# Kernel tuning notes

Hardware: AMD Instinct MI355X
Metric: run time of the kernel (lower is better)

The kernel has to match this reference:

```python
import jax, jax.numpy as jnp
import numpy as np

B = 262144      # batch
DIN = 100       # input covariate dim (cfg_density[0][0])
H = 64          # hidden dim
G = 10          # num_grid -> density output dim G+1
NH = 5          # number of dosage-bucket heads in Multi_head


def setup_inputs() -> dict:
    key = jax.random.key(0)
    ks = jax.random.split(key, 16)
    s = 0.05
    return {
        "dosage": jax.random.uniform(ks[0], (B,), dtype=jnp.float32),
        "x": jax.random.normal(ks[1], (B, DIN), dtype=jnp.float32),
        # density feature MLP (two Linear+ReLU layers)
        "dW0": jax.random.normal(ks[2], (DIN, H), dtype=jnp.float32) * s,
        "db0": jax.random.normal(ks[3], (H,), dtype=jnp.float32) * s,
        "dW1": jax.random.normal(ks[4], (H, H), dtype=jnp.float32) * s,
        "db1": jax.random.normal(ks[5], (H,), dtype=jnp.float32) * s,
        # Density_Block: Linear(H -> G+1) then softmax + grid interpolation
        "dbW": jax.random.normal(ks[6], (H, G + 1), dtype=jnp.float32) * s,
        "dbB": jax.random.normal(ks[7], (G + 1,), dtype=jnp.float32) * s,
        # Multi_head: 5 structurally identical heads, params stacked on axis 0
        # layer0: Treat_Linear(64 -> 64, relu, istreat=1)
        "W0": jax.random.normal(ks[8], (NH, H, H), dtype=jnp.float32) * s,
        "tw0": jax.random.normal(ks[9], (NH, H), dtype=jnp.float32) * s,
        "b0": jax.random.normal(ks[10], (NH, H), dtype=jnp.float32) * s,
        # layer1 (last): Treat_Linear(64 -> 1, no act, istreat=1)
        "W1": jax.random.normal(ks[11], (NH, H, 1), dtype=jnp.float32) * s,
        "tw1": jax.random.normal(ks[12], (NH, 1), dtype=jnp.float32) * s,
        "b1": jax.random.normal(ks[13], (NH, 1), dtype=jnp.float32) * s,
    }


def reference(dosage, x, dW0, db0, dW1, db1, dbW, dbB, W0, tw0, b0, W1, tw1, b1):
    # hidden feature MLP
    hidden = jax.nn.relu(x @ dW0 + db0)
    hidden = jax.nn.relu(hidden @ dW1 + db1)            # [B, H]

    # ---- Density_Block: softmax over grid, dual gather + linear interpolation
    p = jax.nn.softmax(hidden @ dbW + dbB, axis=1)      # [B, G+1]
    tB = dosage * G
    U = jnp.ceil(tB)
    inter = 1.0 - (U - tB)                              # fractional position in cell
    Ui = U.astype(jnp.int32)
    Li = Ui - 1
    Li = Li + (Li < 0).astype(jnp.int32)                # clamp L=-1 -> 0
    pL = jnp.take_along_axis(p, Li[:, None], axis=1)[:, 0]
    pU = jnp.take_along_axis(p, Ui[:, None], axis=1)[:, 0]
    g = pL + (pU - pL) * inter                          # [B]

    # ---- Multi_head: 5 heads on dosage buckets [0,.2),[.2,.4),...,[.8,1.)
    t = dosage
    # layer0: out = feat @ W + t * tw + b, relu; compute all heads, select later
    h0 = jax.nn.relu(
        jnp.einsum('bi,hio->bho', hidden, W0)
        + t[:, None, None] * tw0[None]
        + b0[None]
    )                                                   # [B, NH, H]
    # last layer: no activation
    out1 = (jnp.einsum('bho,hoj->bhj', h0, W1)
            + t[:, None, None] * tw1[None]
            + b1[None])                                 # [B, NH, 1]
    bucket = jnp.clip(jnp.floor(t * NH).astype(jnp.int32), 0, NH - 1)
    Q = jnp.take_along_axis(out1, bucket[:, None, None], axis=1)[:, 0, :]  # [B, 1]
    return g, Q
```

## Files before the change

kernel.cpp:

```cpp
#include <hip/hip_runtime.h>

typedef __attribute__((ext_vector_type(8))) short  short8;
typedef __attribute__((ext_vector_type(4))) float  floatx4;
typedef __attribute__((ext_vector_type(4))) int    intx4;

constexpr int DIN = 100;
constexpr int H   = 64;
constexpr int G   = 10;
constexpr int NH  = 5;
constexpr int MWG = 128;
constexpr int HP  = 72;

constexpr int NF_DW0 = 16, NF_DW1 = 8, NF_DBW = 2;
constexpr int NF_LIN = NF_DW0 + NF_DW1 + NF_DBW;
constexpr int NF_TOT = NF_LIN + 40;

__device__ __forceinline__ unsigned short f2bf_rne(float f) {
    union { float f; unsigned u; } v{f};
    unsigned r = v.u + 0x7FFF + ((v.u >> 16) & 1);
    return (unsigned short)(r >> 16);
}

__device__ __forceinline__ short8 pack8(const float* f) {
    intx4 p;
    #pragma unroll
    for (int j = 0; j < 4; ++j) {
        unsigned a = __float_as_uint(f[2 * j])     + 0x8000u;
        unsigned b = __float_as_uint(f[2 * j + 1]) + 0x8000u;
        p[j] = (int)((b & 0xFFFF0000u) | (a >> 16));
    }
    union { intx4 i; short8 s; } u; u.i = p;
    return u.s;
}

__device__ __forceinline__ unsigned short f2bf_hu(float f) {
    return (unsigned short)((__float_as_uint(f) + 0x8000u) >> 16);
}

__device__ __forceinline__ short8 ldfrag(const unsigned short* __restrict__ ws,
                                         int f, int lane) {
    return *(const short8*)(ws + (size_t)(f * 64 + lane) * 8);
}

__global__ __launch_bounds__(64) void pack_kernel(
    const float* __restrict__ dW0, const float* __restrict__ dW1,
    const float* __restrict__ dbW, const float* __restrict__ W0,
    unsigned short* __restrict__ ws)
{
    const int f = blockIdx.x;
    const int lane = threadIdx.x;
    const int q = lane >> 4, cl = lane & 15;
    float v[8];
    if (f < NF_DW0) {
        int c = f >> 2, g = f & 3;
        #pragma unroll
        for (int j = 0; j < 8; ++j) {
            int k = c * 32 + q * 8 + j, n = g * 16 + cl;
            v[j] = (k < DIN) ? dW0[k * H + n] : 0.0f;
        }
    } else if (f < NF_DW0 + NF_DW1) {
        int r = f - NF_DW0; int c = r >> 2, g = r & 3;
        #pragma unroll
        for (int j = 0; j < 8; ++j) {
            int k = c * 32 + q * 8 + j, n = g * 16 + cl;
            v[j] = dW1[k * H + n];
        }
    } else if (f < NF_LIN) {
        int c = f - (NF_DW0 + NF_DW1);
        #pragma unroll
        for (int j = 0; j < 8; ++j) {
            int k = c * 32 + q * 8 + j, n = cl;
            v[j] = (n <= G) ? dbW[k * (G + 1) + n] : 0.0f;
        }
    } else {
        int r = f - NF_LIN; int h = r >> 3; r &= 7; int c = r >> 2, g = r & 3;
        #pragma unroll
        for (int j = 0; j < 8; ++j) {
            int k = c * 32 + q * 8 + j, n = g * 16 + cl;
            v[j] = W0[(h * H + k) * H + n];
        }
    }
    short8 s;
    #pragma unroll
    for (int j = 0; j < 8; ++j) s[j] = (short)f2bf_rne(v[j]);
    *(short8*)(ws + (size_t)(f * 64 + lane) * 8) = s;
}

__global__ __launch_bounds__(256, 4) void drnet_mfma(
    const float* __restrict__ dosage, const float* __restrict__ x,
    const float* __restrict__ db0, const float* __restrict__ db1,
    const float* __restrict__ dbB,
    const float* __restrict__ tw0, const float* __restrict__ b0,
    const float* __restrict__ W1, const float* __restrict__ tw1,
    const float* __restrict__ b1,
    const unsigned short* __restrict__ wsfrag,
    float* __restrict__ outg, float* __restrict__ outq)
{
    __shared__ unsigned short hbuf[MWG * HP];
    const int tid  = threadIdx.x;
    const int wave = tid >> 6, lane = tid & 63;
    const int q = lane >> 4, cl = lane & 15;
    const int rowbase = blockIdx.x * MWG + wave * 32;
    unsigned short* hb = hbuf + wave * 32 * HP;

    float t8[2][4];
    int   bk8[2][4];
    #pragma unroll
    for (int mt = 0; mt < 2; ++mt) {
        floatx4 tv = *(const floatx4*)(dosage + rowbase + mt * 16 + 4 * q);
        #pragma unroll
        for (int r = 0; r < 4; ++r) {
            float t = tv[r];
            t8[mt][r] = t;
            int bk = (int)floorf(t * (float)NH);
            bk8[mt][r] = min(max(bk, 0), NH - 1);
        }
    }

    #pragma unroll 1
    for (int mt = 0; mt < 2; ++mt) {
        short8 a1[4];
        const float* xr = x + (size_t)(rowbase + mt * 16 + cl) * DIN;
        #pragma unroll
        for (int cch = 0; cch < 4; ++cch) {
            float f[8];
            if (cch < 3) {
                floatx4 u0 = *(const floatx4*)(xr + cch * 32 + q * 8);
                floatx4 u1 = *(const floatx4*)(xr + cch * 32 + q * 8 + 4);
                f[0]=u0.x; f[1]=u0.y; f[2]=u0.z; f[3]=u0.w;
                f[4]=u1.x; f[5]=u1.y; f[6]=u1.z; f[7]=u1.w;
            } else {
                if (q == 0) {
                    floatx4 u0 = *(const floatx4*)(xr + 96);
                    f[0]=u0.x; f[1]=u0.y; f[2]=u0.z; f[3]=u0.w;
                    f[4]=f[5]=f[6]=f[7]=0.0f;
                } else {
                    #pragma unroll
                    for (int j = 0; j < 8; ++j) f[j] = 0.0f;
                }
            }
            a1[cch] = pack8(f);
        }
        floatx4 acc[4];
        #pragma unroll
        for (int g = 0; g < 4; ++g) acc[g] = (floatx4)0.0f;
        #pragma unroll
        for (int cch = 0; cch < 4; ++cch)
            #pragma unroll
            for (int g = 0; g < 4; ++g) {
                short8 bf = ldfrag(wsfrag, cch * 4 + g, lane);
                acc[g] = __builtin_amdgcn_mfma_f32_16x16x32_bf16(a1[cch], bf, acc[g], 0, 0, 0);
            }
        #pragma unroll
        for (int g = 0; g < 4; ++g) {
            float bias = db0[g * 16 + cl];
            #pragma unroll
            for (int r = 0; r < 4; ++r)
                hb[(mt * 16 + 4 * q + r) * HP + g * 16 + cl] =
                    f2bf_hu(fmaxf(acc[g][r] + bias, 0.0f));
        }
    }

    #pragma unroll 1
    for (int mt = 0; mt < 2; ++mt) {
        short8 a2[2];
        #pragma unroll
        for (int cch = 0; cch < 2; ++cch)
            a2[cch] = *(const short8*)(hb + (mt * 16 + cl) * HP + cch * 32 + q * 8);
        floatx4 acc[4];
        #pragma unroll
        for (int g = 0; g < 4; ++g) acc[g] = (floatx4)0.0f;
        #pragma unroll
        for (int cch = 0; cch < 2; ++cch)
            #pragma unroll
            for (int g = 0; g < 4; ++g) {
                short8 bf = ldfrag(wsfrag, NF_DW0 + cch * 4 + g, lane);
                acc[g] = __builtin_amdgcn_mfma_f32_16x16x32_bf16(a2[cch], bf, acc[g], 0, 0, 0);
            }
        #pragma unroll
        for (int g = 0; g < 4; ++g) {
            float bias = db1[g * 16 + cl];
            #pragma unroll
            for (int r = 0; r < 4; ++r)
                hb[(mt * 16 + 4 * q + r) * HP + g * 16 + cl] =
                    f2bf_hu(fmaxf(acc[g][r] + bias, 0.0f));
        }
    }

    short8 af[2][2];
    #pragma unroll
    for (int mt = 0; mt < 2; ++mt)
        #pragma unroll
        for (int cch = 0; cch < 2; ++cch)
            af[mt][cch] = *(const short8*)(hb + (mt * 16 + cl) * HP + cch * 32 + q * 8);

    {
        floatx4 accd[2];
        accd[0] = (floatx4)0.0f; accd[1] = (floatx4)0.0f;
        #pragma unroll
        for (int cch = 0; cch < 2; ++cch) {
            short8 bf = ldfrag(wsfrag, NF_DW0 + NF_DW1 + cch, lane);
            #pragma unroll
            for (int mt = 0; mt < 2; ++mt)
                accd[mt] = __builtin_amdgcn_mfma_f32_16x16x32_bf16(af[mt][cch], bf, accd[mt], 0, 0, 0);
        }
        const float dbBv = (cl <= G) ? dbB[cl] : 0.0f;
        #pragma unroll
        for (int mt = 0; mt < 2; ++mt) {
            float gout[4];
            #pragma unroll
            for (int r = 0; r < 4; ++r) {
                float e = (cl <= G) ? __expf(accd[mt][r] + dbBv) : 0.0f;
                float s = e;
                s += __shfl_xor(s, 1); s += __shfl_xor(s, 2);
                s += __shfl_xor(s, 4); s += __shfl_xor(s, 8);
                const float t  = t8[mt][r];
                const float tB = t * (float)G;
                const float U  = ceilf(tB);
                const float inter = 1.0f - (U - tB);
                int Ui = (int)U; int Li = Ui - 1; if (Li < 0) Li = 0;
                float pL = __shfl(e, q * 16 + Li);
                float pU = __shfl(e, q * 16 + Ui);
                gout[r] = (pL + (pU - pL) * inter) / s;
            }
            if (cl == 0) {
                floatx4 gv = { gout[0], gout[1], gout[2], gout[3] };
                *(floatx4*)(outg + rowbase + mt * 16 + 4 * q) = gv;
            }
        }
    }

    float qp[2][4] = {{0,0,0,0},{0,0,0,0}};
    #pragma unroll 1
    for (int h = 0; h < NH; ++h) {
        #pragma unroll
        for (int gh = 0; gh < 2; ++gh) {
            floatx4 acch[2][2];
            #pragma unroll
            for (int mt = 0; mt < 2; ++mt)
                #pragma unroll
                for (int g = 0; g < 2; ++g) acch[mt][g] = (floatx4)0.0f;
            #pragma unroll
            for (int cch = 0; cch < 2; ++cch)
                #pragma unroll
                for (int g = 0; g < 2; ++g) {
                    short8 bf = ldfrag(wsfrag, NF_LIN + h * 8 + cch * 4 + gh * 2 + g, lane);
                    #pragma unroll
                    for (int mt = 0; mt < 2; ++mt)
                        acch[mt][g] = __builtin_amdgcn_mfma_f32_16x16x32_bf16(af[mt][cch], bf, acch[mt][g], 0, 0, 0);
                }
            #pragma unroll
            for (int g = 0; g < 2; ++g) {
                const int off = h * H + (gh * 2 + g) * 16 + cl;
                const float tw0v = tw0[off], b0v = b0[off], w1v = W1[off];
                #pragma unroll
                for (int mt = 0; mt < 2; ++mt)
                    #pragma unroll
                    for (int r = 0; r < 4; ++r) {
                        float h0 = acch[mt][g][r] + t8[mt][r] * tw0v + b0v;
                        float c  = fmaxf(h0, 0.0f) * w1v;
                        qp[mt][r] += (bk8[mt][r] == h) ? c : 0.0f;
                    }
            }
        }
    }
    #pragma unroll
    for (int mt = 0; mt < 2; ++mt) {
        #pragma unroll
        for (int r = 0; r < 4; ++r) {
            float s = qp[mt][r];
            s += __shfl_xor(s, 1); s += __shfl_xor(s, 2);
            s += __shfl_xor(s, 4); s += __shfl_xor(s, 8);
            const int h = bk8[mt][r];
            qp[mt][r] = s + t8[mt][r] * tw1[h] + b1[h];
        }
        if (cl == 0) {
            floatx4 Qv = { qp[mt][0], qp[mt][1], qp[mt][2], qp[mt][3] };
            *(floatx4*)(outq + rowbase + mt * 16 + 4 * q) = Qv;
        }
    }
}

extern "C" void kernel_launch(void* const* d_in, const int* in_sizes, int n_in,
                              void* d_out, int out_size, void* d_ws, size_t ws_size,
                              hipStream_t stream) {
    const float* dosage = (const float*)d_in[0];
    const float* x      = (const float*)d_in[1];
    const float* dW0    = (const float*)d_in[2];
    const float* db0    = (const float*)d_in[3];
    const float* dW1    = (const float*)d_in[4];
    const float* db1    = (const float*)d_in[5];
    const float* dbW    = (const float*)d_in[6];
    const float* dbB    = (const float*)d_in[7];
    const float* W0     = (const float*)d_in[8];
    const float* tw0    = (const float*)d_in[9];
    const float* b0     = (const float*)d_in[10];
    const float* W1     = (const float*)d_in[11];
    const float* tw1    = (const float*)d_in[12];
    const float* b1     = (const float*)d_in[13];

    const int Btot = in_sizes[0];
    float* outg = (float*)d_out;
    float* outq = outg + Btot;
    unsigned short* ws = (unsigned short*)d_ws;

    pack_kernel<<<NF_TOT, 64, 0, stream>>>(dW0, dW1, dbW, W0, ws);
    drnet_mfma<<<Btot / MWG, 256, 0, stream>>>(dosage, x, db0, db1, dbB,
                                               tw0, b0, W1, tw1, b1,
                                               ws, outg, outq);
}
```

Before: 201.5 us.

## Bucket rows by dosage head so each row evaluates only its own head

Adds a scatter kernel that sorts row indices into per-head lists using shared-memory and global atomics. A new bucketed kernel then processes each head's rows, gathering x rows by index and running only that head's layer-0 MFMAs instead of all five. This removes the redundant head computation, which was the bulk of the MFMA work. In exchange it adds a memset, a scatter pass, non-contiguous gathers and scattered output writes, and it launches many blocks that exit immediately. It falls back to the old kernel when the workspace is too small.

```diff
diff --git a/kernel.cpp b/kernel.cpp
--- a/kernel.cpp
+++ b/kernel.cpp
@@ -84,6 +84,219 @@
     #pragma unroll
     for (int j = 0; j < 8; ++j) s[j] = (short)f2bf_rne(v[j]);
     *(short8*)(ws + (size_t)(f * 64 + lane) * 8) = s;
+}
+
+__global__ __launch_bounds__(256) void scatter_kernel(
+    const float* __restrict__ dosage, int* __restrict__ lists,
+    unsigned* __restrict__ cursors, int Btot)
+{
+    __shared__ unsigned bcnt[NH], gbase[NH];
+    const int tid = threadIdx.x;
+    const int gid = blockIdx.x * 256 + tid;
+    if (tid < NH) bcnt[tid] = 0;
+    __syncthreads();
+    const float t = dosage[gid];
+    int bk = (int)floorf(t * (float)NH);
+    bk = min(max(bk, 0), NH - 1);
+    const unsigned rank = atomicAdd(&bcnt[bk], 1u);
+    __syncthreads();
+    if (tid < NH) gbase[tid] = atomicAdd(&cursors[tid], bcnt[tid]);
+    __syncthreads();
+    lists[(size_t)bk * Btot + gbase[bk] + rank] = gid;
+}
+
+__global__ __launch_bounds__(256, 4) void drnet_bucket(
+    const float* __restrict__ dosage, const float* __restrict__ x,
+    const float* __restrict__ db0, const float* __restrict__ db1,
+    const float* __restrict__ dbB,
+    const float* __restrict__ tw0, const float* __restrict__ b0,
+    const float* __restrict__ W1, const float* __restrict__ tw1,
+    const float* __restrict__ b1,
+    const unsigned short* __restrict__ wsfrag,
+    const int* __restrict__ lists, const unsigned* __restrict__ cursors,
+    float* __restrict__ outg, float* __restrict__ outq,
+    int Btot, int TPB)
+{
+    const int h     = blockIdx.x / TPB;
+    const int tile0 = (blockIdx.x % TPB) * MWG;
+    const int count = (int)cursors[h];
+    if (tile0 >= count) return;
+
+    __shared__ unsigned short hbuf[MWG * HP];
+    const int tid  = threadIdx.x;
+    const int wave = tid >> 6, lane = tid & 63;
+    const int q = lane >> 4, cl = lane & 15;
+    const int wbase = tile0 + wave * 32;
+    if (wbase >= count) return;
+    unsigned short* hb = hbuf + wave * 32 * HP;
+    const int* mylist = lists + (size_t)h * Btot;
+
+    int rowv[2];
+    #pragma unroll
+    for (int mt = 0; mt < 2; ++mt)
+        rowv[mt] = mylist[min(wbase + mt * 16 + cl, count - 1)];
+
+    int   crow[2][4];
+    float t8[2][4];
+    bool  val[2][4];
+    #pragma unroll
+    for (int mt = 0; mt < 2; ++mt)
+        #pragma unroll
+        for (int r = 0; r < 4; ++r) {
+            crow[mt][r] = __shfl(rowv[mt], 20 * q + r);
+            val[mt][r]  = (wbase + mt * 16 + 4 * q + r) < count;
+            t8[mt][r]   = dosage[crow[mt][r]];
+        }
+
+    #pragma unroll 1
+    for (int mt = 0; mt < 2; ++mt) {
+        short8 a1[4];
+        const float* xr = x + (size_t)rowv[mt] * DIN;
+        #pragma unroll
+        for (int cch = 0; cch < 4; ++cch) {
+            float f[8];
+            if (cch < 3) {
+                floatx4 u0 = *(const floatx4*)(xr + cch * 32 + q * 8);
+                floatx4 u1 = *(const floatx4*)(xr + cch * 32 + q * 8 + 4);
+                f[0]=u0.x; f[1]=u0.y; f[2]=u0.z; f[3]=u0.w;
+                f[4]=u1.x; f[5]=u1.y; f[6]=u1.z; f[7]=u1.w;
+            } else {
+                if (q == 0) {
+                    floatx4 u0 = *(const floatx4*)(xr + 96);
+                    f[0]=u0.x; f[1]=u0.y; f[2]=u0.z; f[3]=u0.w;
+                    f[4]=f[5]=f[6]=f[7]=0.0f;
+                } else {
+                    #pragma unroll
+                    for (int j = 0; j < 8; ++j) f[j] = 0.0f;
+                }
+            }
+            a1[cch] = pack8(f);
+        }
+        floatx4 acc[4];
+        #pragma unroll
+        for (int g = 0; g < 4; ++g) acc[g] = (floatx4)0.0f;
+        #pragma unroll
+        for (int cch = 0; cch < 4; ++cch)
+            #pragma unroll
+            for (int g = 0; g < 4; ++g) {
+                short8 bf = ldfrag(wsfrag, cch * 4 + g, lane);
+                acc[g] = __builtin_amdgcn_mfma_f32_16x16x32_bf16(a1[cch], bf, acc[g], 0, 0, 0);
+            }
+        #pragma unroll
+        for (int g = 0; g < 4; ++g) {
+            float bias = db0[g * 16 + cl];
+            #pragma unroll
+            for (int r = 0; r < 4; ++r)
+                hb[(mt * 16 + 4 * q + r) * HP + g * 16 + cl] =
+                    f2bf_hu(fmaxf(acc[g][r] + bias, 0.0f));
+        }
+    }
+
+    #pragma unroll 1
+    for (int mt = 0; mt < 2; ++mt) {
+        short8 a2[2];
+        #pragma unroll
+        for (int cch = 0; cch < 2; ++cch)
+            a2[cch] = *(const short8*)(hb + (mt * 16 + cl) * HP + cch * 32 + q * 8);
+        floatx4 acc[4];
+        #pragma unroll
+        for (int g = 0; g < 4; ++g) acc[g] = (floatx4)0.0f;
+        #pragma unroll
+        for (int cch = 0; cch < 2; ++cch)
+            #pragma unroll
+            for (int g = 0; g < 4; ++g) {
+                short8 bf = ldfrag(wsfrag, NF_DW0 + cch * 4 + g, lane);
+                acc[g] = __builtin_amdgcn_mfma_f32_16x16x32_bf16(a2[cch], bf, acc[g], 0, 0, 0);
+            }
+        #pragma unroll
+        for (int g = 0; g < 4; ++g) {
+            float bias = db1[g * 16 + cl];
+            #pragma unroll
+            for (int r = 0; r < 4; ++r)
+                hb[(mt * 16 + 4 * q + r) * HP + g * 16 + cl] =
+                    f2bf_hu(fmaxf(acc[g][r] + bias, 0.0f));
+        }
+    }
+
+    short8 af[2][2];
+    #pragma unroll
+    for (int mt = 0; mt < 2; ++mt)
+        #pragma unroll
+        for (int cch = 0; cch < 2; ++cch)
+            af[mt][cch] = *(const short8*)(hb + (mt * 16 + cl) * HP + cch * 32 + q * 8);
+
+    {
+        floatx4 accd[2];
+        accd[0] = (floatx4)0.0f; accd[1] = (floatx4)0.0f;
+        #pragma unroll
+        for (int cch = 0; cch < 2; ++cch) {
+            short8 bf = ldfrag(wsfrag, NF_DW0 + NF_DW1 + cch, lane);
+            #pragma unroll
+            for (int mt = 0; mt < 2; ++mt)
+                accd[mt] = __builtin_amdgcn_mfma_f32_16x16x32_bf16(af[mt][cch], bf, accd[mt], 0, 0, 0);
+        }
+        const float dbBv = (cl <= G) ? dbB[cl] : 0.0f;
+        #pragma unroll
+        for (int mt = 0; mt < 2; ++mt) {
+            #pragma unroll
+            for (int r = 0; r < 4; ++r) {
+                float e = (cl <= G) ? __expf(accd[mt][r] + dbBv) : 0.0f;
+                float s = e;
+                s += __shfl_xor(s, 1); s += __shfl_xor(s, 2);
+                s += __shfl_xor(s, 4); s += __shfl_xor(s, 8);
+                const float t  = t8[mt][r];
+                const float tB = t * (float)G;
+                const float U  = ceilf(tB);
+                const float inter = 1.0f - (U - tB);
+                int Ui = (int)U; int Li = Ui - 1; if (Li < 0) Li = 0;
+                float pL = __shfl(e, q * 16 + Li);
+                float pU = __shfl(e, q * 16 + Ui);
+                float gv = (pL + (pU - pL) * inter) / s;
+                if (cl == 0 && val[mt][r]) outg[crow[mt][r]] = gv;
+            }
+        }
+    }
+
+    {
+        floatx4 acch[2][4];
+        #pragma unroll
+        for (int mt = 0; mt < 2; ++mt)
+            #pragma unroll
+            for (int g = 0; g < 4; ++g) acch[mt][g] = (floatx4)0.0f;
+        #pragma unroll
+        for (int cch = 0; cch < 2; ++cch)
+            #pragma unroll
+            for (int g = 0; g < 4; ++g) {
+                short8 bf = ldfrag(wsfrag, NF_LIN + h * 8 + cch * 4 + g, lane);
+                #pragma unroll
+                for (int mt = 0; mt < 2; ++mt)
+                    acch[mt][g] = __builtin_amdgcn_mfma_f32_16x16x32_bf16(af[mt][cch], bf, acch[mt][g], 0, 0, 0);
+            }
+        float qp[2][4] = {{0,0,0,0},{0,0,0,0}};
+        #pragma unroll
+        for (int g = 0; g < 4; ++g) {
+            const int off = h * H + g * 16 + cl;
+            const float tw0v = tw0[off], b0v = b0[off], w1v = W1[off];
+            #pragma unroll
+            for (int mt = 0; mt < 2; ++mt)
+                #pragma unroll
+                for (int r = 0; r < 4; ++r) {
+                    float h0 = acch[mt][g][r] + t8[mt][r] * tw0v + b0v;
+                    qp[mt][r] += fmaxf(h0, 0.0f) * w1v;
+                }
+        }
+        const float tw1v = tw1[h], b1v = b1[h];
+        #pragma unroll
+        for (int mt = 0; mt < 2; ++mt)
+            #pragma unroll
+            for (int r = 0; r < 4; ++r) {
+                float s = qp[mt][r];
+                s += __shfl_xor(s, 1); s += __shfl_xor(s, 2);
+                s += __shfl_xor(s, 4); s += __shfl_xor(s, 8);
+                float qv = s + t8[mt][r] * tw1v + b1v;
+                if (cl == 0 && val[mt][r]) outq[crow[mt][r]] = qv;
+            }
+    }
 }
 
 __global__ __launch_bounds__(256, 4) void drnet_mfma(
@@ -116,7 +329,6 @@
             bk8[mt][r] = min(max(bk, 0), NH - 1);
         }
     }
-
     #pragma unroll 1
     for (int mt = 0; mt < 2; ++mt) {
         short8 a1[4];
@@ -160,7 +372,6 @@
                     f2bf_hu(fmaxf(acc[g][r] + bias, 0.0f));
         }
     }
-
     #pragma unroll 1
     for (int mt = 0; mt < 2; ++mt) {
         short8 a2[2];
@@ -186,14 +397,12 @@
                     f2bf_hu(fmaxf(acc[g][r] + bias, 0.0f));
         }
     }
-
     short8 af[2][2];
     #pragma unroll
     for (int mt = 0; mt < 2; ++mt)
         #pragma unroll
         for (int cch = 0; cch < 2; ++cch)
             af[mt][cch] = *(const short8*)(hb + (mt * 16 + cl) * HP + cch * 32 + q * 8);
-
     {
         floatx4 accd[2];
         accd[0] = (floatx4)0.0f; accd[1] = (floatx4)0.0f;
@@ -229,7 +438,6 @@
             }
         }
     }
-
     float qp[2][4] = {{0,0,0,0},{0,0,0,0}};
     #pragma unroll 1
     for (int h = 0; h < NH; ++h) {
@@ -302,10 +510,26 @@
     const int Btot = in_sizes[0];
     float* outg = (float*)d_out;
     float* outq = outg + Btot;
-    unsigned short* ws = (unsigned short*)d_ws;
-
-    pack_kernel<<<NF_TOT, 64, 0, stream>>>(dW0, dW1, dbW, W0, ws);
-    drnet_mfma<<<Btot / MWG, 256, 0, stream>>>(dosage, x, db0, db1, dbB,
-                                               tw0, b0, W1, tw1, b1,
-                                               ws, outg, outq);
-}
+
+    unsigned short* wsfrag = (unsigned short*)d_ws;
+    const size_t frag_bytes = (size_t)NF_TOT * 64 * 8 * 2;
+    unsigned* cursors = (unsigned*)((char*)d_ws + frag_bytes);
+    int* lists = (int*)((char*)d_ws + frag_bytes + 64);
+    const size_t need = frag_bytes + 64 + (size_t)NH * Btot * 4;
+
+    pack_kernel<<<NF_TOT, 64, 0, stream>>>(dW0, dW1, dbW, W0, wsfrag);
+
+    if (ws_size >= need) {
+        hipMemsetAsync(cursors, 0, NH * sizeof(unsigned), stream);
+        scatter_kernel<<<Btot / 256, 256, 0, stream>>>(dosage, lists, cursors, Btot);
+        const int TPB = Btot / MWG;
+        drnet_bucket<<<NH * TPB, 256, 0, stream>>>(dosage, x, db0, db1, dbB,
+                                                   tw0, b0, W1, tw1, b1,
+                                                   wsfrag, lists, cursors,
+                                                   outg, outq, Btot, TPB);
+    } else {
+        drnet_mfma<<<Btot / MWG, 256, 0, stream>>>(dosage, x, db0, db1, dbB,
+                                                   tw0, b0, W1, tw1, b1,
+                                                   wsfrag, outg, outq);
+    }
+}
```

New measurement: 223.5 us. 1.11x slower.

## Sort rows by dosage bucket per block and skip heads absent in wave

Applied to the files above, without the earlier changes.

Each block counts rows per dosage bucket in shared memory, builds a permutation so each wave processes rows grouped by head, and computes a per-wave bucket mask so head GEMMs are only run for heads present. Head epilogue parameters are pre-packed into float4s in the workspace to cut scalar loads. Rows are gathered and outputs scattered through the permutation, which adds shared-memory atomics, extra barriers and uncoalesced x loads and output stores. With uniform dosage, each 32-row wave likely spans about two heads instead of five.

```diff
diff --git a/kernel.cpp b/kernel.cpp
--- a/kernel.cpp
+++ b/kernel.cpp
@@ -14,6 +14,7 @@
 constexpr int NF_DW0 = 16, NF_DW1 = 8, NF_DBW = 2;
 constexpr int NF_LIN = NF_DW0 + NF_DW1 + NF_DBW;
 constexpr int NF_TOT = NF_LIN + 40;
+constexpr int EPI_F4 = NH * 3 * 16;
 
 __device__ __forceinline__ unsigned short f2bf_rne(float f) {
     union { float f; unsigned u; } v{f};
@@ -45,11 +46,27 @@
 __global__ __launch_bounds__(64) void pack_kernel(
     const float* __restrict__ dW0, const float* __restrict__ dW1,
     const float* __restrict__ dbW, const float* __restrict__ W0,
-    unsigned short* __restrict__ ws)
+    const float* __restrict__ tw0, const float* __restrict__ b0,
+    const float* __restrict__ W1,
+    unsigned short* __restrict__ ws, float* __restrict__ wsepi)
 {
     const int f = blockIdx.x;
     const int lane = threadIdx.x;
     const int q = lane >> 4, cl = lane & 15;
+    if (f == NF_TOT) {
+        for (int idx = lane; idx < EPI_F4; idx += 64) {
+            const int h = idx / 48, rem = idx % 48;
+            const int which = rem / 16, c = rem % 16;
+            const float* src = (which == 0) ? tw0 : (which == 1) ? b0 : W1;
+            float4 v;
+            v.x = src[h * H + 0 * 16 + c];
+            v.y = src[h * H + 1 * 16 + c];
+            v.z = src[h * H + 2 * 16 + c];
+            v.w = src[h * H + 3 * 16 + c];
+            *(float4*)(wsepi + idx * 4) = v;
+        }
+        return;
+    }
     float v[8];
     if (f < NF_DW0) {
         int c = f >> 2, g = f & 3;
@@ -86,41 +103,70 @@
     *(short8*)(ws + (size_t)(f * 64 + lane) * 8) = s;
 }
 
-__global__ __launch_bounds__(256, 4) void drnet_mfma(
+__global__ __launch_bounds__(256, 4) void drnet_sorted(
     const float* __restrict__ dosage, const float* __restrict__ x,
     const float* __restrict__ db0, const float* __restrict__ db1,
     const float* __restrict__ dbB,
-    const float* __restrict__ tw0, const float* __restrict__ b0,
-    const float* __restrict__ W1, const float* __restrict__ tw1,
-    const float* __restrict__ b1,
+    const float* __restrict__ tw1, const float* __restrict__ b1,
     const unsigned short* __restrict__ wsfrag,
+    const floatx4* __restrict__ wsepi,
     float* __restrict__ outg, float* __restrict__ outq)
 {
     __shared__ unsigned short hbuf[MWG * HP];
+    __shared__ int      perm[MWG];
+    __shared__ unsigned scnt[8];
+    __shared__ unsigned sbase[8];
+
     const int tid  = threadIdx.x;
     const int wave = tid >> 6, lane = tid & 63;
     const int q = lane >> 4, cl = lane & 15;
-    const int rowbase = blockIdx.x * MWG + wave * 32;
+    const int rowbase = blockIdx.x * MWG;
     unsigned short* hb = hbuf + wave * 32 * HP;
 
-    float t8[2][4];
-    int   bk8[2][4];
+    if (tid < 8) scnt[tid] = 0;
+    __syncthreads();
+    int mybk = 0; unsigned myrank = 0;
+    if (tid < MWG) {
+        float t = dosage[rowbase + tid];
+        mybk = min(max((int)floorf(t * (float)NH), 0), NH - 1);
+        myrank = atomicAdd(&scnt[mybk], 1u);
+    }
+    __syncthreads();
+    if (tid == 0) {
+        unsigned s = 0;
+        #pragma unroll
+        for (int h = 0; h < NH; ++h) { sbase[h] = s; s += scnt[h]; }
+    }
+    __syncthreads();
+    if (tid < MWG) perm[sbase[mybk] + myrank] = tid;
+    __syncthreads();
+
+    int li[2]; float tl[2]; int bkl[2];
     #pragma unroll
     for (int mt = 0; mt < 2; ++mt) {
-        floatx4 tv = *(const floatx4*)(dosage + rowbase + mt * 16 + 4 * q);
+        li[mt]  = perm[wave * 32 + mt * 16 + cl];
+        tl[mt]  = dosage[rowbase + li[mt]];
+        bkl[mt] = min(max((int)floorf(tl[mt] * (float)NH), 0), NH - 1);
+    }
+    unsigned mk = (1u << bkl[0]) | (1u << bkl[1]);
+    mk |= __shfl_xor(mk, 1); mk |= __shfl_xor(mk, 2);
+    mk |= __shfl_xor(mk, 4); mk |= __shfl_xor(mk, 8);
+    const unsigned mku = (unsigned)__builtin_amdgcn_readfirstlane((int)mk);
+
+    int crow[2][4]; float t8[2][4]; int bk8[2][4];
+    #pragma unroll
+    for (int mt = 0; mt < 2; ++mt)
         #pragma unroll
         for (int r = 0; r < 4; ++r) {
-            float t = tv[r];
-            t8[mt][r] = t;
-            int bk = (int)floorf(t * (float)NH);
-            bk8[mt][r] = min(max(bk, 0), NH - 1);
-        }
-    }
+            crow[mt][r] = __shfl(li[mt],  20 * q + r);
+            t8[mt][r]   = __shfl(tl[mt],  20 * q + r);
+            bk8[mt][r]  = __shfl(bkl[mt], 20 * q + r);
+        }
 
     #pragma unroll 1
     for (int mt = 0; mt < 2; ++mt) {
         short8 a1[4];
-        const float* xr = x + (size_t)(rowbase + mt * 16 + cl) * DIN;
+        const float* xr = x + (size_t)(rowbase + li[mt]) * DIN;
         #pragma unroll
         for (int cch = 0; cch < 4; ++cch) {
             float f[8];
@@ -206,8 +252,7 @@
         }
         const float dbBv = (cl <= G) ? dbB[cl] : 0.0f;
         #pragma unroll
-        for (int mt = 0; mt < 2; ++mt) {
-            float gout[4];
+        for (int mt = 0; mt < 2; ++mt)
             #pragma unroll
             for (int r = 0; r < 4; ++r) {
                 float e = (cl <= G) ? __expf(accd[mt][r] + dbBv) : 0.0f;
@@ -221,64 +266,56 @@
                 int Ui = (int)U; int Li = Ui - 1; if (Li < 0) Li = 0;
                 float pL = __shfl(e, q * 16 + Li);
                 float pU = __shfl(e, q * 16 + Ui);
-                gout[r] = (pL + (pU - pL) * inter) / s;
-            }
-            if (cl == 0) {
-                floatx4 gv = { gout[0], gout[1], gout[2], gout[3] };
-                *(floatx4*)(outg + rowbase + mt * 16 + 4 * q) = gv;
-            }
-        }
+                float gv = (pL + (pU - pL) * inter) / s;
+                if (cl == 0) outg[rowbase + crow[mt][r]] = gv;
+            }
     }
 
     float qp[2][4] = {{0,0,0,0},{0,0,0,0}};
     #pragma unroll 1
     for (int h = 0; h < NH; ++h) {
-        #pragma unroll
-        for (int gh = 0; gh < 2; ++gh) {
-            floatx4 acch[2][2];
-            #pragma unroll
-            for (int mt = 0; mt < 2; ++mt)
-                #pragma unroll
-                for (int g = 0; g < 2; ++g) acch[mt][g] = (floatx4)0.0f;
-            #pragma unroll
-            for (int cch = 0; cch < 2; ++cch)
-                #pragma unroll
-                for (int g = 0; g < 2; ++g) {
-                    short8 bf = ldfrag(wsfrag, NF_LIN + h * 8 + cch * 4 + gh * 2 + g, lane);
-                    #pragma unroll
-                    for (int mt = 0; mt < 2; ++mt)
-                        acch[mt][g] = __builtin_amdgcn_mfma_f32_16x16x32_bf16(af[mt][cch], bf, acch[mt][g], 0, 0, 0);
-                }
-            #pragma unroll
-            for (int g = 0; g < 2; ++g) {
-                const int off = h * H + (gh * 2 + g) * 16 + cl;
-                const float tw0v = tw0[off], b0v = b0[off], w1v = W1[off];
+        if (!((mku >> h) & 1u)) continue;
+        floatx4 acch[2][4];
+        #pragma unroll
+        for (int mt = 0; mt < 2; ++mt)
+            #pragma unroll
+            for (int g = 0; g < 4; ++g) acch[mt][g] = (floatx4)0.0f;
+        #pragma unroll
+        for (int cch = 0; cch < 2; ++cch)
+            #pragma unroll
+            for (int g = 0; g < 4; ++g) {
+                short8 bf = ldfrag(wsfrag, NF_LIN + h * 8 + cch * 4 + g, lane);
                 #pragma unroll
                 for (int mt = 0; mt < 2; ++mt)
-                    #pragma unroll
-                    for (int r = 0; r < 4; ++r) {
-                        float h0 = acch[mt][g][r] + t8[mt][r] * tw0v + b0v;
-                        float c  = fmaxf(h0, 0.0f) * w1v;
-                        qp[mt][r] += (bk8[mt][r] == h) ? c : 0.0f;
-                    }
-            }
-        }
-    }
-    #pragma unroll
-    for (int mt = 0; mt < 2; ++mt) {
+                    acch[mt][g] = __builtin_amdgcn_mfma_f32_16x16x32_bf16(af[mt][cch], bf, acch[mt][g], 0, 0, 0);
+            }
+        const floatx4 tw0v = wsepi[(h * 3 + 0) * 16 + cl];
+        const floatx4 b0v  = wsepi[(h * 3 + 1) * 16 + cl];
+        const floatx4 w1v  = wsepi[(h * 3 + 2) * 16 + cl];
+        #pragma unroll
+        for (int mt = 0; mt < 2; ++mt)
+            #pragma unroll
+            for (int r = 0; r < 4; ++r) {
+                float s = 0.0f;
+                #pragma unroll
+                for (int g = 0; g < 4; ++g) {
+                    float h0 = acch[mt][g][r] + t8[mt][r] * tw0v[g] + b0v[g];
+                    s += fmaxf(h0, 0.0f) * w1v[g];
+                }
+                qp[mt][r] += (bk8[mt][r] == h) ? s : 0.0f;
+            }
+    }
+    #pragma unroll
+    for (int mt = 0; mt < 2; ++mt)
         #pragma unroll
         for (int r = 0; r < 4; ++r) {
             float s = qp[mt][r];
             s += __shfl_xor(s, 1); s += __shfl_xor(s, 2);
             s += __shfl_xor(s, 4); s += __shfl_xor(s, 8);
             const int h = bk8[mt][r];
-            qp[mt][r] = s + t8[mt][r] * tw1[h] + b1[h];
-        }
-        if (cl == 0) {
-            floatx4 Qv = { qp[mt][0], qp[mt][1], qp[mt][2], qp[mt][3] };
-            *(floatx4*)(outq + rowbase + mt * 16 + 4 * q) = Qv;
-        }
-    }
+            float qv = s + t8[mt][r] * tw1[h] + b1[h];
+            if (cl == 0) outq[rowbase + crow[mt][r]] = qv;
+        }
 }
 
 extern "C" void kernel_launch(void* const* d_in, const int* in_sizes, int n_in,
@@ -302,10 +339,15 @@
     const int Btot = in_sizes[0];
     float* outg = (float*)d_out;
     float* outq = outg + Btot;
-    unsigned short* ws = (unsigned short*)d_ws;
-
-    pack_kernel<<<NF_TOT, 64, 0, stream>>>(dW0, dW1, dbW, W0, ws);
-    drnet_mfma<<<Btot / MWG, 256, 0, stream>>>(dosage, x, db0, db1, dbB,
-                                               tw0, b0, W1, tw1, b1,
-                                               ws, outg, outq);
-}
+
+    unsigned short* wsfrag = (unsigned short*)d_ws;
+    const size_t frag_bytes = (size_t)NF_TOT * 64 * 8 * 2;
+    float* wsepi = (float*)((char*)d_ws + frag_bytes);
+
+    pack_kernel<<<NF_TOT + 1, 64, 0, stream>>>(dW0, dW1, dbW, W0, tw0, b0, W1,
+                                               wsfrag, wsepi);
+    drnet_sorted<<<Btot / MWG, 256, 0, stream>>>(dosage, x, db0, db1, dbB,
+                                                 tw1, b1, wsfrag,
+                                                 (const floatx4*)wsepi,
+                                                 outg, outq);
+}
```

New measurement: 209.9 us. +4.2%, slower.
